# Kernel tuning notes

Measured on AMD Instinct MI355X. Metric: run time of the kernel, lower is better.

Reference implementation:

```python
import jax, jax.numpy as jnp
import numpy as np

N_ROWS = 524288   # total ragged rows (sum of lengths)
N_SEG = 128       # number of segments (batch of ragged sequences)
N_FEAT = 256      # num_features
EPS = 1e-05


def setup_inputs() -> dict:
    key = jax.random.key(0)
    k_x = jax.random.fold_in(key, 1)
    x = jax.random.normal(k_x, (N_ROWS, N_FEAT), dtype=jnp.float32)
    # ragged lengths: strictly positive, sum exactly N_ROWS
    rng = np.random.default_rng(0)
    boundaries = np.sort(rng.choice(np.arange(1, N_ROWS), size=N_SEG - 1, replace=False))
    lengths_np = np.diff(np.concatenate([[0], boundaries, [N_ROWS]])).astype(np.int64)
    lengths = jnp.asarray(lengths_np)
    weight = jnp.ones((N_FEAT,), dtype=jnp.float32)
    bias = jnp.zeros((N_FEAT,), dtype=jnp.float32)
    return {"x": x, "lengths": lengths, "weight": weight, "bias": bias}


def reference(x, lengths, weight, bias):
    # instance norm over ragged segments: per-segment, per-feature mean/var
    B = lengths.shape[0]
    seg_ids = jnp.repeat(jnp.arange(B, dtype=jnp.int32), lengths,
                         total_repeat_length=x.shape[0])      # [N]
    cnt = lengths.astype(x.dtype)[:, None]                    # [B,1]
    mean = jax.ops.segment_sum(x, seg_ids, num_segments=B) / cnt          # [B,F]
    x_centered = x - mean[seg_ids]                                        # [N,F]
    var = jax.ops.segment_sum(x_centered * x_centered, seg_ids,
                              num_segments=B) / cnt                       # [B,F]
    std = jnp.sqrt(var + EPS)                                             # [B,F]
    x_norm = x_centered / std[seg_ids]                                    # [N,F]
    return x_norm * weight + bias
```

## Files before the change

kernel.cpp:

```cpp
#include <hip/hip_runtime.h>
#include <hip/hip_bf16.h>

#define NFEAT 256
#define NQ    64
#define CH    256
#define BLK   256

typedef float f32x4_native __attribute__((ext_vector_type(4)));

__device__ __forceinline__ void nt_store4(float4* p, float4 v) {
    f32x4_native n; n.x = v.x; n.y = v.y; n.z = v.z; n.w = v.w;
    __builtin_nontemporal_store(n, reinterpret_cast<f32x4_native*>(p));
}

__global__ __launch_bounds__(BLK) void k_setup(const int* __restrict__ lengths, int B,
                                               int* __restrict__ off, int* __restrict__ bs,
                                               int* __restrict__ nblk) {
    __shared__ int L[BLK], C[BLK];
    const int t = threadIdx.x;
    int len = (t < B) ? lengths[t] : 0;
    L[t] = len;
    C[t] = (len + CH - 1) / CH;
    __syncthreads();
    for (int d = 1; d < BLK; d <<= 1) {
        int a = L[t], c = C[t], aa = 0, cc = 0;
        if (t >= d) { aa = L[t - d]; cc = C[t - d]; }
        __syncthreads();
        L[t] = a + aa; C[t] = c + cc;
        __syncthreads();
    }
    if (t == 0) { off[0] = 0; bs[0] = 0; }
    if (t < B)  { off[t + 1] = L[t]; bs[t + 1] = C[t]; }
    if (t == B - 1) *nblk = C[t];
}

__device__ __forceinline__ int find_seg(const int* __restrict__ bs, int B, int bid) {
    __shared__ int sseg;
    const int t = threadIdx.x;
    if (t < B && bs[t] <= bid && bid < bs[t + 1]) sseg = t;
    __syncthreads();
    return sseg;
}

__global__ __launch_bounds__(BLK) void k_partial(const float* __restrict__ x,
                                                 const int* __restrict__ off,
                                                 const int* __restrict__ bs,
                                                 const int* __restrict__ nblk,
                                                 int B,
                                                 float* __restrict__ psum,
                                                 float* __restrict__ psumsq) {
    const int bid = blockIdx.x;
    if (bid >= *nblk) return;

    const int seg = find_seg(bs, B, bid);
    const int r0 = off[seg] + (bid - bs[seg]) * CH;
    const int r1 = min(r0 + CH, off[seg + 1]);

    const int rl = threadIdx.x >> 6;
    const int q  = threadIdx.x & 63;

    float4 sum = make_float4(0.f, 0.f, 0.f, 0.f);
    float4 sq  = make_float4(0.f, 0.f, 0.f, 0.f);

    const float4* x4 = reinterpret_cast<const float4*>(x);
    #pragma unroll 8
    for (int r = r0 + rl; r < r1; r += 4) {
        float4 v = x4[(size_t)r * NQ + q];
        sum.x += v.x; sum.y += v.y; sum.z += v.z; sum.w += v.w;
        sq.x  += v.x * v.x; sq.y += v.y * v.y; sq.z += v.z * v.z; sq.w += v.w * v.w;
    }

    __shared__ float4 lsum[4][NQ];
    __shared__ float4 lsq[4][NQ];
    lsum[rl][q] = sum;
    lsq[rl][q]  = sq;
    __syncthreads();

    if (rl == 0) {
        float4 a0 = lsum[0][q], a1 = lsum[1][q], a2 = lsum[2][q], a3 = lsum[3][q];
        float4 q0 = lsq[0][q],  q1 = lsq[1][q],  q2 = lsq[2][q],  q3 = lsq[3][q];
        float4 ts, tq;
        ts.x = a0.x + a1.x + a2.x + a3.x;  ts.y = a0.y + a1.y + a2.y + a3.y;
        ts.z = a0.z + a1.z + a2.z + a3.z;  ts.w = a0.w + a1.w + a2.w + a3.w;
        tq.x = q0.x + q1.x + q2.x + q3.x;  tq.y = q0.y + q1.y + q2.y + q3.y;
        tq.z = q0.z + q1.z + q2.z + q3.z;  tq.w = q0.w + q1.w + q2.w + q3.w;
        reinterpret_cast<float4*>(psum)[(size_t)bid * NQ + q]   = ts;
        reinterpret_cast<float4*>(psumsq)[(size_t)bid * NQ + q] = tq;
    }
}

__global__ __launch_bounds__(BLK) void k_finalize(const float* __restrict__ psum,
                                                  const float* __restrict__ psumsq,
                                                  const int* __restrict__ off,
                                                  const int* __restrict__ bs,
                                                  const float* __restrict__ weight,
                                                  const float* __restrict__ bias,
                                                  float* __restrict__ scale,
                                                  float* __restrict__ shift) {
    const int seg = blockIdx.x;
    const int f   = threadIdx.x;
    const int b0 = bs[seg], b1 = bs[seg + 1];
    float s = 0.f, qq = 0.f;
    for (int b = b0; b < b1; ++b) {
        s  += psum[(size_t)b * NFEAT + f];
        qq += psumsq[(size_t)b * NFEAT + f];
    }
    const float cnt  = (float)(off[seg + 1] - off[seg]);
    const float m    = s / cnt;
    const float var  = fmaxf(qq / cnt - m * m, 0.f);
    const float rstd = rsqrtf(var + 1e-5f);
    const float sc   = rstd * weight[f];
    scale[(size_t)seg * NFEAT + f] = sc;
    shift[(size_t)seg * NFEAT + f] = bias[f] - m * sc;
}

__global__ __launch_bounds__(BLK) void k_norm(const float* __restrict__ x,
                                              const int* __restrict__ off,
                                              const int* __restrict__ bs,
                                              const int* __restrict__ nblk,
                                              int B,
                                              const float* __restrict__ scale,
                                              const float* __restrict__ shift,
                                              float* __restrict__ out) {
    const int bid = blockIdx.x;
    if (bid >= *nblk) return;

    const int seg = find_seg(bs, B, bid);
    const int r0 = off[seg] + (bid - bs[seg]) * CH;
    const int r1 = min(r0 + CH, off[seg + 1]);

    const int rl = threadIdx.x >> 6;
    const int q  = threadIdx.x & 63;

    const float4 sc = reinterpret_cast<const float4*>(scale)[(size_t)seg * NQ + q];
    const float4 sh = reinterpret_cast<const float4*>(shift)[(size_t)seg * NQ + q];

    const float4* x4 = reinterpret_cast<const float4*>(x);
    float4* o4 = reinterpret_cast<float4*>(out);
    #pragma unroll 8
    for (int r = r0 + rl; r < r1; r += 4) {
        const size_t idx = (size_t)r * NQ + q;
        float4 v = x4[idx];
        float4 o;
        o.x = v.x * sc.x + sh.x;
        o.y = v.y * sc.y + sh.y;
        o.z = v.z * sc.z + sh.z;
        o.w = v.w * sc.w + sh.w;
        nt_store4(&o4[idx], o);
    }
}

extern "C" void kernel_launch(void* const* d_in, const int* in_sizes, int n_in,
                              void* d_out, int out_size, void* d_ws, size_t ws_size,
                              hipStream_t stream) {
    const float* x       = (const float*)d_in[0];
    const int*   lengths = (const int*)d_in[1];
    const float* weight  = (const float*)d_in[2];
    const float* bias    = (const float*)d_in[3];
    float*       out     = (float*)d_out;

    const int B = in_sizes[1];
    const int N = in_sizes[0] / NFEAT;
    const int maxCh = N / CH + B;

    char* ws = (char*)d_ws;
    int*   off    = (int*)ws;
    int*   bs     = off + 160;
    int*   nblk   = bs + 160;
    float* scale  = (float*)(ws + 4096);
    float* shift  = scale + (size_t)B * NFEAT;
    float* psum   = shift + (size_t)B * NFEAT;
    float* psumsq = psum + (size_t)maxCh * NFEAT;

    k_setup<<<1, BLK, 0, stream>>>(lengths, B, off, bs, nblk);
    k_partial<<<maxCh, BLK, 0, stream>>>(x, off, bs, nblk, B, psum, psumsq);
    k_finalize<<<B, BLK, 0, stream>>>(psum, psumsq, off, bs, weight, bias, scale, shift);
    k_norm<<<maxCh, BLK, 0, stream>>>(x, off, bs, nblk, B, scale, shift, out);
}
```

Before: 352.5 us.

## Fuse statistics and normalization into one kernel with LDS staging and per-segment flags

Replaces the partial, finalize and normalize kernels with a single kernel. Each block stages its 64-row chunk of x in shared memory while reducing partial sums. The last block of each segment, found with an atomic counter, computes scale and shift and raises a flag. All blocks spin on that flag, then normalize from shared memory, so x is read from HBM once instead of twice and two launches disappear. In exchange it uses about 64KB of LDS per block, which limits occupancy. It also depends on every block of a segment being resident at once, so the spin-wait could hang if dispatch order or residency does not allow that.

```diff
diff --git a/kernel.cpp b/kernel.cpp
--- a/kernel.cpp
+++ b/kernel.cpp
@@ -1,9 +1,8 @@
 #include <hip/hip_runtime.h>
-#include <hip/hip_bf16.h>
 
 #define NFEAT 256
 #define NQ    64
-#define CH    256
+#define CH    64
 #define BLK   256
 
 typedef float f32x4_native __attribute__((ext_vector_type(4)));
@@ -15,7 +14,7 @@
 
 __global__ __launch_bounds__(BLK) void k_setup(const int* __restrict__ lengths, int B,
                                                int* __restrict__ off, int* __restrict__ bs,
-                                               int* __restrict__ nblk) {
+                                               int* __restrict__ cnt, int* __restrict__ flag) {
     __shared__ int L[BLK], C[BLK];
     const int t = threadIdx.x;
     int len = (t < B) ? lengths[t] : 0;
@@ -30,55 +29,55 @@
         __syncthreads();
     }
     if (t == 0) { off[0] = 0; bs[0] = 0; }
-    if (t < B)  { off[t + 1] = L[t]; bs[t + 1] = C[t]; }
-    if (t == B - 1) *nblk = C[t];
+    if (t < B)  { off[t + 1] = L[t]; bs[t + 1] = C[t]; cnt[t] = 0; flag[t] = 0; }
 }
 
-__device__ __forceinline__ int find_seg(const int* __restrict__ bs, int B, int bid) {
-    __shared__ int sseg;
-    const int t = threadIdx.x;
-    if (t < B && bs[t] <= bid && bid < bs[t + 1]) sseg = t;
+__global__ __launch_bounds__(BLK) void k_main(
+    const float* __restrict__ x,
+    const float* __restrict__ weight, const float* __restrict__ bias,
+    float* __restrict__ out,
+    const int* __restrict__ off, const int* __restrict__ bs, int B,
+    float* __restrict__ psum, float* __restrict__ psumsq,
+    float* __restrict__ scale, float* __restrict__ shift,
+    int* __restrict__ cnt, int* __restrict__ flag)
+{
+    const int t   = threadIdx.x;
+    const int bid = blockIdx.x;
+
+    __shared__ int soff[132], sbs[132];
+    __shared__ int sseg, is_last;
+    if (t <= B) { soff[t] = off[t]; sbs[t] = bs[t]; }
     __syncthreads();
-    return sseg;
-}
+    if (bid >= sbs[B]) return;
 
-__global__ __launch_bounds__(BLK) void k_partial(const float* __restrict__ x,
-                                                 const int* __restrict__ off,
-                                                 const int* __restrict__ bs,
-                                                 const int* __restrict__ nblk,
-                                                 int B,
-                                                 float* __restrict__ psum,
-                                                 float* __restrict__ psumsq) {
-    const int bid = blockIdx.x;
-    if (bid >= *nblk) return;
+    if (t < B && sbs[t] <= bid && bid < sbs[t + 1]) sseg = t;
+    __syncthreads();
+    const int seg = sseg;
+    const int r0 = soff[seg] + (bid - sbs[seg]) * CH;
+    const int r1 = min(r0 + CH, soff[seg + 1]);
 
-    const int seg = find_seg(bs, B, bid);
-    const int r0 = off[seg] + (bid - bs[seg]) * CH;
-    const int r1 = min(r0 + CH, off[seg + 1]);
+    const int rl = t >> 6;
+    const int q  = t & 63;
 
-    const int rl = threadIdx.x >> 6;
-    const int q  = threadIdx.x & 63;
+    __shared__ float4 stage[CH * NQ];
+    __shared__ float4 red[2][4][NQ];
 
     float4 sum = make_float4(0.f, 0.f, 0.f, 0.f);
     float4 sq  = make_float4(0.f, 0.f, 0.f, 0.f);
-
     const float4* x4 = reinterpret_cast<const float4*>(x);
     #pragma unroll 8
     for (int r = r0 + rl; r < r1; r += 4) {
         float4 v = x4[(size_t)r * NQ + q];
+        stage[((r - r0) << 6) | q] = v;
         sum.x += v.x; sum.y += v.y; sum.z += v.z; sum.w += v.w;
         sq.x  += v.x * v.x; sq.y += v.y * v.y; sq.z += v.z * v.z; sq.w += v.w * v.w;
     }
-
-    __shared__ float4 lsum[4][NQ];
-    __shared__ float4 lsq[4][NQ];
-    lsum[rl][q] = sum;
-    lsq[rl][q]  = sq;
+    red[0][rl][q] = sum;
+    red[1][rl][q] = sq;
     __syncthreads();
-
     if (rl == 0) {
-        float4 a0 = lsum[0][q], a1 = lsum[1][q], a2 = lsum[2][q], a3 = lsum[3][q];
-        float4 q0 = lsq[0][q],  q1 = lsq[1][q],  q2 = lsq[2][q],  q3 = lsq[3][q];
+        float4 a0 = red[0][0][q], a1 = red[0][1][q], a2 = red[0][2][q], a3 = red[0][3][q];
+        float4 q0 = red[1][0][q], q1 = red[1][1][q], q2 = red[1][2][q], q3 = red[1][3][q];
         float4 ts, tq;
         ts.x = a0.x + a1.x + a2.x + a3.x;  ts.y = a0.y + a1.y + a2.y + a3.y;
         ts.z = a0.z + a1.z + a2.z + a3.z;  ts.w = a0.w + a1.w + a2.w + a3.w;
@@ -87,66 +86,55 @@
         reinterpret_cast<float4*>(psum)[(size_t)bid * NQ + q]   = ts;
         reinterpret_cast<float4*>(psumsq)[(size_t)bid * NQ + q] = tq;
     }
-}
+    __syncthreads();
 
-__global__ __launch_bounds__(BLK) void k_finalize(const float* __restrict__ psum,
-                                                  const float* __restrict__ psumsq,
-                                                  const int* __restrict__ off,
-                                                  const int* __restrict__ bs,
-                                                  const float* __restrict__ weight,
-                                                  const float* __restrict__ bias,
-                                                  float* __restrict__ scale,
-                                                  float* __restrict__ shift) {
-    const int seg = blockIdx.x;
-    const int f   = threadIdx.x;
-    const int b0 = bs[seg], b1 = bs[seg + 1];
-    float s = 0.f, qq = 0.f;
-    for (int b = b0; b < b1; ++b) {
-        s  += psum[(size_t)b * NFEAT + f];
-        qq += psumsq[(size_t)b * NFEAT + f];
+    if (t == 0) {
+        int old = __hip_atomic_fetch_add(&cnt[seg], 1,
+                                         __ATOMIC_RELEASE, __HIP_MEMORY_SCOPE_AGENT);
+        is_last = (old == (sbs[seg + 1] - sbs[seg] - 1));
     }
-    const float cnt  = (float)(off[seg + 1] - off[seg]);
-    const float m    = s / cnt;
-    const float var  = fmaxf(qq / cnt - m * m, 0.f);
-    const float rstd = rsqrtf(var + 1e-5f);
-    const float sc   = rstd * weight[f];
-    scale[(size_t)seg * NFEAT + f] = sc;
-    shift[(size_t)seg * NFEAT + f] = bias[f] - m * sc;
-}
+    __syncthreads();
 
-__global__ __launch_bounds__(BLK) void k_norm(const float* __restrict__ x,
-                                              const int* __restrict__ off,
-                                              const int* __restrict__ bs,
-                                              const int* __restrict__ nblk,
-                                              int B,
-                                              const float* __restrict__ scale,
-                                              const float* __restrict__ shift,
-                                              float* __restrict__ out) {
-    const int bid = blockIdx.x;
-    if (bid >= *nblk) return;
+    if (is_last) {
+        (void)__hip_atomic_load(&cnt[seg], __ATOMIC_ACQUIRE, __HIP_MEMORY_SCOPE_AGENT);
+        float s = 0.f, qq = 0.f;
+        const int b0 = sbs[seg], b1 = sbs[seg + 1];
+        for (int b = b0; b < b1; ++b) {
+            s  += psum[(size_t)b * NFEAT + t];
+            qq += psumsq[(size_t)b * NFEAT + t];
+        }
+        const float cf   = (float)(soff[seg + 1] - soff[seg]);
+        const float m    = s / cf;
+        const float var  = fmaxf(qq / cf - m * m, 0.f);
+        const float rstd = rsqrtf(var + 1e-5f);
+        const float sc_  = rstd * weight[t];
+        scale[(size_t)seg * NFEAT + t] = sc_;
+        shift[(size_t)seg * NFEAT + t] = bias[t] - m * sc_;
+        __syncthreads();
+        if (t == 0)
+            __hip_atomic_store(&flag[seg], 1, __ATOMIC_RELEASE, __HIP_MEMORY_SCOPE_AGENT);
+    }
 
-    const int seg = find_seg(bs, B, bid);
-    const int r0 = off[seg] + (bid - bs[seg]) * CH;
-    const int r1 = min(r0 + CH, off[seg + 1]);
-
-    const int rl = threadIdx.x >> 6;
-    const int q  = threadIdx.x & 63;
+    if (t == 0) {
+        while (__hip_atomic_load(&flag[seg], __ATOMIC_RELAXED,
+                                 __HIP_MEMORY_SCOPE_AGENT) == 0)
+            __builtin_amdgcn_s_sleep(2);
+        (void)__hip_atomic_load(&flag[seg], __ATOMIC_ACQUIRE, __HIP_MEMORY_SCOPE_AGENT);
+    }
+    __syncthreads();
 
     const float4 sc = reinterpret_cast<const float4*>(scale)[(size_t)seg * NQ + q];
     const float4 sh = reinterpret_cast<const float4*>(shift)[(size_t)seg * NQ + q];
-
-    const float4* x4 = reinterpret_cast<const float4*>(x);
     float4* o4 = reinterpret_cast<float4*>(out);
     #pragma unroll 8
     for (int r = r0 + rl; r < r1; r += 4) {
-        const size_t idx = (size_t)r * NQ + q;
-        float4 v = x4[idx];
+        float4 v = stage[((r - r0) << 6) | q];
         float4 o;
         o.x = v.x * sc.x + sh.x;
         o.y = v.y * sc.y + sh.y;
         o.z = v.z * sc.z + sh.z;
         o.w = v.w * sc.w + sh.w;
-        nt_store4(&o4[idx], o);
+        nt_store4(&o4[(size_t)r * NQ + q], o);
     }
 }
 
@@ -166,14 +154,14 @@
     char* ws = (char*)d_ws;
     int*   off    = (int*)ws;
     int*   bs     = off + 160;
-    int*   nblk   = bs + 160;
-    float* scale  = (float*)(ws + 4096);
+    int*   cnt    = bs + 160;
+    int*   flag   = cnt + 160;
+    float* scale  = (float*)(ws + 8192);
     float* shift  = scale + (size_t)B * NFEAT;
     float* psum   = shift + (size_t)B * NFEAT;
     float* psumsq = psum + (size_t)maxCh * NFEAT;
 
-    k_setup<<<1, BLK, 0, stream>>>(lengths, B, off, bs, nblk);
-    k_partial<<<maxCh, BLK, 0, stream>>>(x, off, bs, nblk, B, psum, psumsq);
-    k_finalize<<<B, BLK, 0, stream>>>(psum, psumsq, off, bs, weight, bias, scale, shift);
-    k_norm<<<maxCh, BLK, 0, stream>>>(x, off, bs, nblk, B, scale, shift, out);
+    k_setup<<<1, BLK, 0, stream>>>(lengths, B, off, bs, cnt, flag);
+    k_main<<<maxCh, BLK, 0, stream>>>(x, weight, bias, out, off, bs, B,
+                                      psum, psumsq, scale, shift, cnt, flag);
 }
```

Result: slower. 1.003 ms (+184.5%).

## Fold segment scan into each kernel, reverse norm block order, unroll finalize

Applied to the files above, without the earlier changes.

Drops the separate single-block setup kernel; each block of the partial, finalize and norm kernels recomputes the prefix scan of lengths in shared memory. This removes one launch and a serialized dependency, at the cost of redundant scan work per block. The norm kernel now walks chunks in reverse so the chunks read last by the partial pass, likely still in cache, are processed first. Finalize uses four independent accumulators to expose more memory-level parallelism.

```diff
diff --git a/kernel.cpp b/kernel.cpp
--- a/kernel.cpp
+++ b/kernel.cpp
@@ -1,5 +1,4 @@
 #include <hip/hip_runtime.h>
-#include <hip/hip_bf16.h>
 
 #define NFEAT 256
 #define NQ    64
@@ -13,15 +12,15 @@
     __builtin_nontemporal_store(n, reinterpret_cast<f32x4_native*>(p));
 }
 
-__global__ __launch_bounds__(BLK) void k_setup(const int* __restrict__ lengths, int B,
-                                               int* __restrict__ off, int* __restrict__ bs,
-                                               int* __restrict__ nblk) {
+__device__ __forceinline__ void block_scan(const int* __restrict__ lengths, int B,
+                                           int* soff, int* sbs) {
     __shared__ int L[BLK], C[BLK];
     const int t = threadIdx.x;
     int len = (t < B) ? lengths[t] : 0;
     L[t] = len;
     C[t] = (len + CH - 1) / CH;
     __syncthreads();
+    #pragma unroll
     for (int d = 1; d < BLK; d <<= 1) {
         int a = L[t], c = C[t], aa = 0, cc = 0;
         if (t >= d) { aa = L[t - d]; cc = C[t - d]; }
@@ -29,35 +28,37 @@
         L[t] = a + aa; C[t] = c + cc;
         __syncthreads();
     }
-    if (t == 0) { off[0] = 0; bs[0] = 0; }
-    if (t < B)  { off[t + 1] = L[t]; bs[t + 1] = C[t]; }
-    if (t == B - 1) *nblk = C[t];
+    if (t == 0) { soff[0] = 0; sbs[0] = 0; }
+    if (t < B)  { soff[t + 1] = L[t]; sbs[t + 1] = C[t]; }
+    __syncthreads();
 }
 
-__device__ __forceinline__ int find_seg(const int* __restrict__ bs, int B, int bid) {
+__device__ __forceinline__ int find_seg(const int* __restrict__ sbs, int B, int c) {
     __shared__ int sseg;
     const int t = threadIdx.x;
-    if (t < B && bs[t] <= bid && bid < bs[t + 1]) sseg = t;
+    if (t < B && sbs[t] <= c && c < sbs[t + 1]) sseg = t;
     __syncthreads();
     return sseg;
 }
 
 __global__ __launch_bounds__(BLK) void k_partial(const float* __restrict__ x,
-                                                 const int* __restrict__ off,
-                                                 const int* __restrict__ bs,
-                                                 const int* __restrict__ nblk,
+                                                 const int* __restrict__ lengths,
                                                  int B,
                                                  float* __restrict__ psum,
                                                  float* __restrict__ psumsq) {
+    __shared__ int soff[132], sbs[132];
+    block_scan(lengths, B, soff, sbs);
+
     const int bid = blockIdx.x;
-    if (bid >= *nblk) return;
+    if (bid >= sbs[B]) return;
 
-    const int seg = find_seg(bs, B, bid);
-    const int r0 = off[seg] + (bid - bs[seg]) * CH;
-    const int r1 = min(r0 + CH, off[seg + 1]);
+    const int seg = find_seg(sbs, B, bid);
+    const int r0 = soff[seg] + (bid - sbs[seg]) * CH;
+    const int r1 = min(r0 + CH, soff[seg + 1]);
 
-    const int rl = threadIdx.x >> 6;
-    const int q  = threadIdx.x & 63;
+    const int t  = threadIdx.x;
+    const int rl = t >> 6;
+    const int q  = t & 63;
 
     float4 sum = make_float4(0.f, 0.f, 0.f, 0.f);
     float4 sq  = make_float4(0.f, 0.f, 0.f, 0.f);
@@ -91,21 +92,36 @@
 
 __global__ __launch_bounds__(BLK) void k_finalize(const float* __restrict__ psum,
                                                   const float* __restrict__ psumsq,
-                                                  const int* __restrict__ off,
-                                                  const int* __restrict__ bs,
+                                                  const int* __restrict__ lengths,
+                                                  int B,
                                                   const float* __restrict__ weight,
                                                   const float* __restrict__ bias,
                                                   float* __restrict__ scale,
                                                   float* __restrict__ shift) {
+    __shared__ int soff[132], sbs[132];
+    block_scan(lengths, B, soff, sbs);
+
     const int seg = blockIdx.x;
     const int f   = threadIdx.x;
-    const int b0 = bs[seg], b1 = bs[seg + 1];
-    float s = 0.f, qq = 0.f;
-    for (int b = b0; b < b1; ++b) {
-        s  += psum[(size_t)b * NFEAT + f];
-        qq += psumsq[(size_t)b * NFEAT + f];
+    const int b0 = sbs[seg], b1 = sbs[seg + 1];
+
+    float s0 = 0.f, s1 = 0.f, s2 = 0.f, s3 = 0.f;
+    float q0 = 0.f, q1 = 0.f, q2 = 0.f, q3 = 0.f;
+    int b = b0;
+    for (; b + 3 < b1; b += 4) {
+        s0 += psum[(size_t)(b + 0) * NFEAT + f];  q0 += psumsq[(size_t)(b + 0) * NFEAT + f];
+        s1 += psum[(size_t)(b + 1) * NFEAT + f];  q1 += psumsq[(size_t)(b + 1) * NFEAT + f];
+        s2 += psum[(size_t)(b + 2) * NFEAT + f];  q2 += psumsq[(size_t)(b + 2) * NFEAT + f];
+        s3 += psum[(size_t)(b + 3) * NFEAT + f];  q3 += psumsq[(size_t)(b + 3) * NFEAT + f];
     }
-    const float cnt  = (float)(off[seg + 1] - off[seg]);
+    for (; b < b1; ++b) {
+        s0 += psum[(size_t)b * NFEAT + f];
+        q0 += psumsq[(size_t)b * NFEAT + f];
+    }
+    const float s  = (s0 + s1) + (s2 + s3);
+    const float qq = (q0 + q1) + (q2 + q3);
+
+    const float cnt  = (float)(soff[seg + 1] - soff[seg]);
     const float m    = s / cnt;
     const float var  = fmaxf(qq / cnt - m * m, 0.f);
     const float rstd = rsqrtf(var + 1e-5f);
@@ -115,22 +131,25 @@
 }
 
 __global__ __launch_bounds__(BLK) void k_norm(const float* __restrict__ x,
-                                              const int* __restrict__ off,
-                                              const int* __restrict__ bs,
-                                              const int* __restrict__ nblk,
+                                              const int* __restrict__ lengths,
                                               int B,
                                               const float* __restrict__ scale,
                                               const float* __restrict__ shift,
                                               float* __restrict__ out) {
-    const int bid = blockIdx.x;
-    if (bid >= *nblk) return;
+    __shared__ int soff[132], sbs[132];
+    block_scan(lengths, B, soff, sbs);
 
-    const int seg = find_seg(bs, B, bid);
-    const int r0 = off[seg] + (bid - bs[seg]) * CH;
-    const int r1 = min(r0 + CH, off[seg + 1]);
+    const int nch = sbs[B];
+    if ((int)blockIdx.x >= nch) return;
+    const int c = nch - 1 - blockIdx.x;
 
-    const int rl = threadIdx.x >> 6;
-    const int q  = threadIdx.x & 63;
+    const int seg = find_seg(sbs, B, c);
+    const int r0 = soff[seg] + (c - sbs[seg]) * CH;
+    const int r1 = min(r0 + CH, soff[seg + 1]);
+
+    const int t  = threadIdx.x;
+    const int rl = t >> 6;
+    const int q  = t & 63;
 
     const float4 sc = reinterpret_cast<const float4*>(scale)[(size_t)seg * NQ + q];
     const float4 sh = reinterpret_cast<const float4*>(shift)[(size_t)seg * NQ + q];
@@ -164,16 +183,12 @@
     const int maxCh = N / CH + B;
 
     char* ws = (char*)d_ws;
-    int*   off    = (int*)ws;
-    int*   bs     = off + 160;
-    int*   nblk   = bs + 160;
     float* scale  = (float*)(ws + 4096);
     float* shift  = scale + (size_t)B * NFEAT;
     float* psum   = shift + (size_t)B * NFEAT;
     float* psumsq = psum + (size_t)maxCh * NFEAT;
 
-    k_setup<<<1, BLK, 0, stream>>>(lengths, B, off, bs, nblk);
-    k_partial<<<maxCh, BLK, 0, stream>>>(x, off, bs, nblk, B, psum, psumsq);
-    k_finalize<<<B, BLK, 0, stream>>>(psum, psumsq, off, bs, weight, bias, scale, shift);
-    k_norm<<<maxCh, BLK, 0, stream>>>(x, off, bs, nblk, B, scale, shift, out);
+    k_partial<<<maxCh, BLK, 0, stream>>>(x, lengths, B, psum, psumsq);
+    k_finalize<<<B, BLK, 0, stream>>>(psum, psumsq, lengths, B, weight, bias, scale, shift);
+    k_norm<<<maxCh, BLK, 0, stream>>>(x, lengths, B, scale, shift, out);
 }
```

Result: faster. 301.9 us (median of 3 runs) (-14.4%).
